# Optimization experiments

Measured on AMD Instinct MI355X. Metric: run time of the kernel, lower is better.

The kernel has to match this reference:

```python
import jax, jax.numpy as jnp
import numpy as np

GRID = 192
ISO = 0.0

CORNERS = [(0,0,0),(1,0,0),(0,1,0),(1,1,0),(0,0,1),(1,0,1),(0,1,1),(1,1,1)]
# 12 cube edges as pairs of corner offsets
EDGES = [
    ((0,0,0),(1,0,0)),((0,1,0),(1,1,0)),((0,0,1),(1,0,1)),((0,1,1),(1,1,1)),
    ((0,0,0),(0,1,0)),((1,0,0),(1,1,0)),((0,0,1),(0,1,1)),((1,0,1),(1,1,1)),
    ((0,0,0),(0,0,1)),((1,0,0),(1,0,1)),((0,1,0),(0,1,1)),((1,1,0),(1,1,1)),
]


def setup_inputs() -> dict:
    key = jax.random.key(0)
    grid = jax.random.normal(key, (GRID, GRID, GRID), dtype=jnp.float32)
    return {"grid": grid}


def _dual_verts(grid, iso):
    # One dual vertex per cell of the padded grid: mean of the iso-crossing
    # points on the cell's 12 edges (dual-marching-cubes vertex placement).
    X, Y, Z = grid.shape
    P = jnp.pad(grid, 1, constant_values=iso + 1.0)  # (X+2, Y+2, Z+2)
    Cx, Cy, Cz = X + 1, Y + 1, Z + 1                 # number of cells per axis
    vals = {c: P[c[0]:c[0]+Cx, c[1]:c[1]+Cy, c[2]:c[2]+Cz] for c in CORNERS}
    sum_pt = jnp.zeros((Cx, Cy, Cz, 3), grid.dtype)
    cnt = jnp.zeros((Cx, Cy, Cz), grid.dtype)
    for ca, cb in EDGES:  # fixed 12-iteration loop, fully vectorized over cells
        vA, vB = vals[ca], vals[cb]
        m = (vA < iso) != (vB < iso)                 # edge crosses isosurface
        t = jnp.where(m, (iso - vA) / jnp.where(m, vB - vA, 1.0), 0.0)
        oa = jnp.asarray(ca, grid.dtype)
        ob = jnp.asarray(cb, grid.dtype)
        pt = oa + t[..., None] * (ob - oa)           # local crossing point
        mf = m.astype(grid.dtype)
        sum_pt = sum_pt + mf[..., None] * pt
        cnt = cnt + mf
    base = jnp.stack(jnp.meshgrid(jnp.arange(Cx), jnp.arange(Cy), jnp.arange(Cz), indexing='ij'), axis=-1).astype(grid.dtype)
    verts = base + sum_pt / jnp.maximum(cnt, 1.0)[..., None]
    # undo +1 padding offset, then normalize by (dim - 1) as in the module
    verts = (verts - 1.0) / (jnp.asarray([X, Y, Z], grid.dtype) - 1.0)
    return verts.reshape(-1, 3), (cnt > 0).reshape(-1)


def _quads(grid, iso):
    # One quad per grid edge that crosses the isosurface, connecting the dual
    # vertices of the 4 cells sharing that edge. Emitted densely with a mask
    # (jit-compatible fixed shapes); masked rows are inactive.
    X, Y, Z = grid.shape
    P = jnp.pad(grid, 1, constant_values=iso + 1.0)
    Cx, Cy, Cz = X + 1, Y + 1, Z + 1
    sgn = P < iso
    def cid(a, b, c):  # flatten cell index
        return (a * Cy + b) * Cz + c
    qs, ms = [], []
    # x-directed edges: shared by cells (i, j-1/j, k-1/k)
    m = sgn[0:Cx, 1:Cy, 1:Cz] != sgn[1:Cx+1, 1:Cy, 1:Cz]
    a = jnp.arange(Cx)[:, None, None]; b = jnp.arange(1, Cy)[None, :, None]; c = jnp.arange(1, Cz)[None, None, :]
    q = jnp.stack(jnp.broadcast_arrays(cid(a, b-1, c-1), cid(a, b, c-1), cid(a, b, c), cid(a, b-1, c)), axis=-1)
    qs.append(q.reshape(-1, 4)); ms.append(m.reshape(-1))
    # y-directed edges: shared by cells (i-1/i, j, k-1/k)
    m = sgn[1:Cx, 0:Cy, 1:Cz] != sgn[1:Cx, 1:Cy+1, 1:Cz]
    a = jnp.arange(1, Cx)[:, None, None]; b = jnp.arange(Cy)[None, :, None]; c = jnp.arange(1, Cz)[None, None, :]
    q = jnp.stack(jnp.broadcast_arrays(cid(a-1, b, c-1), cid(a, b, c-1), cid(a, b, c), cid(a-1, b, c)), axis=-1)
    qs.append(q.reshape(-1, 4)); ms.append(m.reshape(-1))
    # z-directed edges: shared by cells (i-1/i, j-1/j, k)
    m = sgn[1:Cx, 1:Cy, 0:Cz] != sgn[1:Cx, 1:Cy, 1:Cz+1]
    a = jnp.arange(1, Cx)[:, None, None]; b = jnp.arange(1, Cy)[None, :, None]; c = jnp.arange(Cz)[None, None, :]
    q = jnp.stack(jnp.broadcast_arrays(cid(a-1, b-1, c), cid(a, b-1, c), cid(a, b, c), cid(a-1, b, c)), axis=-1)
    qs.append(q.reshape(-1, 4)); ms.append(m.reshape(-1))
    quads = jnp.concatenate(qs, axis=0).astype(jnp.int32)
    qmask = jnp.concatenate(ms, axis=0)
    return quads, qmask


def reference(grid):
    verts, vmask = _dual_verts(grid, ISO)
    quads, qmask = _quads(grid, ISO)
    return verts, vmask, quads, qmask
```

## Files before the change

kernel.cpp:

```cpp
#include <hip/hip_runtime.h>

#define GN 192
#define CN 193
#define CN2 (CN * CN)

#define NV        ((size_t)CN * CN * CN)
#define OFF_VMASK ((size_t)(NV * 3))
#define OFF_QUADS ((size_t)(OFF_VMASK + NV))
#define QSEG      ((size_t)CN * GN * GN)
#define OFF_QMASK ((size_t)(OFF_QUADS + 3 * QSEG * 4))

typedef float f4 __attribute__((ext_vector_type(4)));

__device__ __forceinline__ void nts(float* p, float v) { __builtin_nontemporal_store(v, p); }
__device__ __forceinline__ void nts4(f4* p, f4 v) { __builtin_nontemporal_store(v, p); }

#define QBLK 6948

__global__ __launch_bounds__(256) void dmc_quads(float* __restrict__ out) {
    f4* const quads = (f4*)(out + OFF_QUADS);
    const unsigned b = blockIdx.x;
    const unsigned seg = b / QBLK;
    const unsigned r0 = (b - seg * QBLK) * 1024u + threadIdx.x;
    float d0, d1, d2, d3;
    if (seg == 0)      { d0 = 0.f;      d1 = 193.f;  d2 = 194.f; d3 = 1.f; }
    else if (seg == 1) { d0 = -37249.f; d1 = 0.f;    d2 = 1.f;   d3 = -37248.f; }
    else               { d0 = -37442.f; d1 = -193.f; d2 = 0.f;   d3 = -37249.f; }
#pragma unroll
    for (int s = 0; s < 4; ++s) {
        const unsigned r = r0 + 256u * s;
        unsigned i, j, k, t;
        if (seg == 0)      { k = r % GN; t = r / GN; j = t % GN; i = t / GN; }
        else if (seg == 1) { k = r % GN; t = r / GN; j = t % CN; i = t / CN + 1; }
        else               { k = r % CN; t = r / CN; j = t % GN + 1; i = t / GN + 1; }
        const float flin = (float)((i * CN + j) * CN + k);
        nts4(quads + seg * QSEG + r, (f4){flin + d0, flin + d1, flin + d2, flin + d3});
    }
}

__global__ __launch_bounds__(256) void dmc_verts(const float* __restrict__ g,
                                                 float* __restrict__ out) {
    __shared__ __align__(16) float vlds[256 * 3];
    __shared__ float qAl[256], qBl[256], qCl[256];

    const int tid = threadIdx.x;
    const size_t lin0 = (size_t)blockIdx.x * 256;
    const size_t lin = lin0 + tid;
    const bool valid = lin < NV;
    const int linI = valid ? (int)lin : (int)(NV - 1);
    const int k = linI % CN;
    const int t2 = linI / CN;
    const int j = t2 % CN;
    const int i = t2 / CN;

    const int L0 = (int)lin0;
    const int L1 = (int)((lin0 + 255 < NV) ? (lin0 + 255) : (NV - 1));
    const int k0 = L0 % CN, u0 = L0 / CN, j0 = u0 % CN, i0 = u0 / CN;
    const int k1 = L1 % CN, u1 = L1 / CN, j1 = u1 % CN, i1 = u1 / CN;

    int rminA, rmaxA, rminB, rmaxB, rminC, rmaxC;
    { int a = i0, bb = j0, c = k0;
      if (bb == GN) { a++; bb = 0; c = 0; }
      else if (c == GN) { bb++; c = 0; if (bb == GN) { a++; bb = 0; } }
      rminA = (a * GN + bb) * GN + c; }
    { int a = i1, bb = j1, c = k1;
      if (bb == GN) { bb = GN - 1; c = GN - 1; }
      else if (c == GN) { c = GN - 1; }
      rmaxA = (a * GN + bb) * GN + c; }
    { int a = i0, bb = j0, c = k0;
      if (a == 0) { a = 1; bb = 0; c = 0; }
      else if (c == GN) { bb++; c = 0; if (bb == CN) { bb = 0; a++; } }
      rminB = ((a - 1) * CN + bb) * GN + c; }
    { int a = i1, bb = j1, c = k1;
      if (a == 0) rmaxB = -1;
      else { if (c == GN) c = GN - 1; rmaxB = ((a - 1) * CN + bb) * GN + c; } }
    { int a = i0, bb = j0, c = k0;
      if (a == 0) { a = 1; bb = 1; c = 0; }
      else if (bb == 0) { bb = 1; c = 0; }
      rminC = ((a - 1) * GN + (bb - 1)) * CN + c; }
    { int a = i1, bb = j1, c = k1;
      if (a == 0) rmaxC = -1;
      else if (bb == 0) { a--; rmaxC = (a == 0) ? -1 : ((a - 1) * GN + (GN - 1)) * CN + (CN - 1); }
      else rmaxC = ((a - 1) * GN + (bb - 1)) * CN + c; }
    int cntA = rmaxA - rminA + 1; if (cntA < 0) cntA = 0;
    int cntB = rmaxB - rminB + 1; if (cntB < 0) cntB = 0;
    int cntC = rmaxC - rminC + 1; if (cntC < 0) cntC = 0;

    const int xm = (i >= 1) ? i - 1 : 0;
    const int xp = (i <= GN - 1) ? i : GN - 1;
    const int ym = (j >= 1) ? j - 1 : 0;
    const int yp = (j <= GN - 1) ? j : GN - 1;
    const int zm = (k >= 1) ? k - 1 : 0;
    const int zp = (k <= GN - 1) ? k : GN - 1;
    const bool xv0 = (i >= 1), xv1 = (i <= GN - 1);
    const bool yv0 = (j >= 1), yv1 = (j <= GN - 1);
    const bool zv0 = (k >= 1), zv1 = (k <= GN - 1);

    const float* b00 = g + ((size_t)xm * GN + ym) * GN;
    const float* b01 = g + ((size_t)xm * GN + yp) * GN;
    const float* b10 = g + ((size_t)xp * GN + ym) * GN;
    const float* b11 = g + ((size_t)xp * GN + yp) * GN;

    const float v000 = (xv0 & yv0 & zv0) ? b00[zm] : 1.0f;
    const float v001 = (xv0 & yv0 & zv1) ? b00[zp] : 1.0f;
    const float v010 = (xv0 & yv1 & zv0) ? b01[zm] : 1.0f;
    const float v011 = (xv0 & yv1 & zv1) ? b01[zp] : 1.0f;
    const float v100 = (xv1 & yv0 & zv0) ? b10[zm] : 1.0f;
    const float v101 = (xv1 & yv0 & zv1) ? b10[zp] : 1.0f;
    const float v110 = (xv1 & yv1 & zv0) ? b11[zm] : 1.0f;
    const float v111 = (xv1 & yv1 & zv1) ? b11[zp] : 1.0f;

    float sx = 0.f, sy = 0.f, sz = 0.f, cf = 0.f;
    auto acc = [&](float vA, float vB, int axis, float o1, float o2) {
        const bool cr = (vA < 0.f) != (vB < 0.f);
        const float m = cr ? 1.0f : 0.0f;
        const float d = cr ? (vB - vA) : 1.0f;
        float r = __builtin_amdgcn_rcpf(d);
        r = r * (2.0f - d * r);
        const float t = cr ? (-vA * r) : 0.0f;
        if (axis == 0)      { sx += t;      sy += m * o1; sz += m * o2; }
        else if (axis == 1) { sx += m * o1; sy += t;      sz += m * o2; }
        else                { sx += m * o1; sy += m * o2; sz += t;      }
        cf += m;
    };
    acc(v000, v100, 0, 0.f, 0.f);
    acc(v010, v110, 0, 1.f, 0.f);
    acc(v001, v101, 0, 0.f, 1.f);
    acc(v011, v111, 0, 1.f, 1.f);
    acc(v000, v010, 1, 0.f, 0.f);
    acc(v100, v110, 1, 1.f, 0.f);
    acc(v001, v011, 1, 0.f, 1.f);
    acc(v101, v111, 1, 1.f, 1.f);
    acc(v000, v001, 2, 0.f, 0.f);
    acc(v100, v101, 2, 1.f, 0.f);
    acc(v010, v011, 2, 0.f, 1.f);
    acc(v110, v111, 2, 1.f, 1.f);

    const float cfm = fmaxf(cf, 1.0f);
    float rc = __builtin_amdgcn_rcpf(cfm);
    rc = rc * (2.0f - cfm * rc);
    const float inv191 = 1.0f / 191.0f;
    vlds[tid * 3 + 0] = ((float)i + sx * rc - 1.0f) * inv191;
    vlds[tid * 3 + 1] = ((float)j + sy * rc - 1.0f) * inv191;
    vlds[tid * 3 + 2] = ((float)k + sz * rc - 1.0f) * inv191;

    if (valid) nts(out + OFF_VMASK + lin, (cf > 0.f) ? 1.0f : 0.0f);

    if (valid) {
        if (j < GN && k < GN)
            qAl[(i * GN + j) * GN + k - rminA] = ((v011 < 0.f) != (v111 < 0.f)) ? 1.0f : 0.0f;
        if (i >= 1 && k < GN)
            qBl[((i - 1) * CN + j) * GN + k - rminB] = ((v001 < 0.f) != (v011 < 0.f)) ? 1.0f : 0.0f;
        if (i >= 1 && j >= 1)
            qCl[((i - 1) * GN + (j - 1)) * CN + k - rminC] = ((v000 < 0.f) != (v001 < 0.f)) ? 1.0f : 0.0f;
    }
    __syncthreads();

    const int nvalid = L1 - L0 + 1;
    const int nfl = 3 * nvalid;
    const int nf4 = nfl >> 2;
    if (tid < nf4)
        nts4((f4*)(out + lin0 * 3) + tid, ((const f4*)vlds)[tid]);
    if (tid == nf4)
        for (int rr = nf4 * 4; rr < nfl; ++rr) nts(out + lin0 * 3 + rr, vlds[rr]);

    if (tid < cntA) nts(out + OFF_QMASK + (size_t)rminA + tid, qAl[tid]);
    if (tid < cntB) nts(out + OFF_QMASK + QSEG + (size_t)rminB + tid, qBl[tid]);
    if (tid < cntC) nts(out + OFF_QMASK + 2 * QSEG + (size_t)rminC + tid, qCl[tid]);
}

extern "C" void kernel_launch(void* const* d_in, const int* in_sizes, int n_in,
                              void* d_out, int out_size, void* d_ws, size_t ws_size,
                              hipStream_t stream) {
    const float* g = (const float*)d_in[0];
    float* out = (float*)d_out;
    const int nbV = (int)((NV + 255) / 256);
    dmc_verts<<<dim3(nbV), dim3(256), 0, stream>>>(g, out);
    dmc_quads<<<dim3(3 * QBLK), dim3(256), 0, stream>>>(out);
}
```

Before: 573.5 us.

## Fuse vertex and quad kernels into persistent row-wise kernel with LDS double buffering

Replaces the separate vertex and quad kernels with one persistent kernel in which each block handles whole (i,j) rows of cells. The four input grid rows a row needs are staged into LDS with the next row prefetched into a second buffer, and vertices, masks, quad indices and quad masks are all written directly from that row. This removes the second launch, the redundant per-cell global gathers and the LDS repacking of mask outputs. In exchange, vertex output now uses scalar strided stores instead of packed float4 stores, and 256 threads cover only 193 cells, so about a quarter of the lanes sit idle in the compute phase.

```diff
diff --git a/kernel.cpp b/kernel.cpp
--- a/kernel.cpp
+++ b/kernel.cpp
@@ -2,7 +2,7 @@
 
 #define GN 192
 #define CN 193
-#define CN2 (CN * CN)
+#define NROWS (CN * CN)
 
 #define NV        ((size_t)CN * CN * CN)
 #define OFF_VMASK ((size_t)(NV * 3))
@@ -15,158 +15,125 @@
 __device__ __forceinline__ void nts(float* p, float v) { __builtin_nontemporal_store(v, p); }
 __device__ __forceinline__ void nts4(f4* p, f4 v) { __builtin_nontemporal_store(v, p); }
 
-#define QBLK 6948
+#define NBLK 4096
 
-__global__ __launch_bounds__(256) void dmc_quads(float* __restrict__ out) {
-    f4* const quads = (f4*)(out + OFF_QUADS);
-    const unsigned b = blockIdx.x;
-    const unsigned seg = b / QBLK;
-    const unsigned r0 = (b - seg * QBLK) * 1024u + threadIdx.x;
-    float d0, d1, d2, d3;
-    if (seg == 0)      { d0 = 0.f;      d1 = 193.f;  d2 = 194.f; d3 = 1.f; }
-    else if (seg == 1) { d0 = -37249.f; d1 = 0.f;    d2 = 1.f;   d3 = -37248.f; }
-    else               { d0 = -37442.f; d1 = -193.f; d2 = 0.f;   d3 = -37249.f; }
-#pragma unroll
-    for (int s = 0; s < 4; ++s) {
-        const unsigned r = r0 + 256u * s;
-        unsigned i, j, k, t;
-        if (seg == 0)      { k = r % GN; t = r / GN; j = t % GN; i = t / GN; }
-        else if (seg == 1) { k = r % GN; t = r / GN; j = t % CN; i = t / CN + 1; }
-        else               { k = r % CN; t = r / CN; j = t % GN + 1; i = t / GN + 1; }
-        const float flin = (float)((i * CN + j) * CN + k);
-        nts4(quads + seg * QSEG + r, (f4){flin + d0, flin + d1, flin + d2, flin + d3});
+__global__ __launch_bounds__(256) void dmc_rows(const float* __restrict__ g,
+                                                float* __restrict__ out) {
+    __shared__ float rows[2][4][194];
+    const int tid = threadIdx.x;
+
+    if (tid < 16) rows[tid >> 3][(tid >> 1) & 3][(tid & 1) * 193] = 1.0f;
+
+    const int  rsel   = tid / 48;
+    const int  f4i    = tid - rsel * 48;
+    const bool stager = tid < 192;
+
+    unsigned row = blockIdx.x;
+
+    if (row < NROWS && stager) {
+        const int i = row / CN, j = row - (row / CN) * CN;
+        const int gx = i - 1 + (rsel >> 1);
+        const int gy = j - 1 + (rsel & 1);
+        f4 v = (f4){1.f, 1.f, 1.f, 1.f};
+        if ((unsigned)gx < GN && (unsigned)gy < GN)
+            v = ((const f4*)(g + ((size_t)gx * GN + gy) * GN))[f4i];
+        float* d = &rows[0][rsel][1 + 4 * f4i];
+        d[0] = v.x; d[1] = v.y; d[2] = v.z; d[3] = v.w;
     }
-}
 
-__global__ __launch_bounds__(256) void dmc_verts(const float* __restrict__ g,
-                                                 float* __restrict__ out) {
-    __shared__ __align__(16) float vlds[256 * 3];
-    __shared__ float qAl[256], qBl[256], qCl[256];
+    int buf = 0;
+    for (; row < NROWS; row += NBLK) {
+        __syncthreads();
 
-    const int tid = threadIdx.x;
-    const size_t lin0 = (size_t)blockIdx.x * 256;
-    const size_t lin = lin0 + tid;
-    const bool valid = lin < NV;
-    const int linI = valid ? (int)lin : (int)(NV - 1);
-    const int k = linI % CN;
-    const int t2 = linI / CN;
-    const int j = t2 % CN;
-    const int i = t2 / CN;
+        const unsigned nrow = row + NBLK;
+        const bool havenext = (nrow < NROWS) && stager;
+        f4 nxt = (f4){1.f, 1.f, 1.f, 1.f};
+        if (havenext) {
+            const int ni = nrow / CN, nj = nrow - (nrow / CN) * CN;
+            const int gx = ni - 1 + (rsel >> 1);
+            const int gy = nj - 1 + (rsel & 1);
+            if ((unsigned)gx < GN && (unsigned)gy < GN)
+                nxt = ((const f4*)(g + ((size_t)gx * GN + gy) * GN))[f4i];
+        }
 
-    const int L0 = (int)lin0;
-    const int L1 = (int)((lin0 + 255 < NV) ? (lin0 + 255) : (NV - 1));
-    const int k0 = L0 % CN, u0 = L0 / CN, j0 = u0 % CN, i0 = u0 / CN;
-    const int k1 = L1 % CN, u1 = L1 / CN, j1 = u1 % CN, i1 = u1 / CN;
+        const int i = row / CN;
+        const int j = row - i * CN;
+        const int k = tid;
+        if (k < CN) {
+            const float* r00 = rows[buf][0];
+            const float* r01 = rows[buf][1];
+            const float* r10 = rows[buf][2];
+            const float* r11 = rows[buf][3];
+            const float v000 = r00[k], v001 = r00[k + 1];
+            const float v010 = r01[k], v011 = r01[k + 1];
+            const float v100 = r10[k], v101 = r10[k + 1];
+            const float v110 = r11[k], v111 = r11[k + 1];
 
-    int rminA, rmaxA, rminB, rmaxB, rminC, rmaxC;
-    { int a = i0, bb = j0, c = k0;
-      if (bb == GN) { a++; bb = 0; c = 0; }
-      else if (c == GN) { bb++; c = 0; if (bb == GN) { a++; bb = 0; } }
-      rminA = (a * GN + bb) * GN + c; }
-    { int a = i1, bb = j1, c = k1;
-      if (bb == GN) { bb = GN - 1; c = GN - 1; }
-      else if (c == GN) { c = GN - 1; }
-      rmaxA = (a * GN + bb) * GN + c; }
-    { int a = i0, bb = j0, c = k0;
-      if (a == 0) { a = 1; bb = 0; c = 0; }
-      else if (c == GN) { bb++; c = 0; if (bb == CN) { bb = 0; a++; } }
-      rminB = ((a - 1) * CN + bb) * GN + c; }
-    { int a = i1, bb = j1, c = k1;
-      if (a == 0) rmaxB = -1;
-      else { if (c == GN) c = GN - 1; rmaxB = ((a - 1) * CN + bb) * GN + c; } }
-    { int a = i0, bb = j0, c = k0;
-      if (a == 0) { a = 1; bb = 1; c = 0; }
-      else if (bb == 0) { bb = 1; c = 0; }
-      rminC = ((a - 1) * GN + (bb - 1)) * CN + c; }
-    { int a = i1, bb = j1, c = k1;
-      if (a == 0) rmaxC = -1;
-      else if (bb == 0) { a--; rmaxC = (a == 0) ? -1 : ((a - 1) * GN + (GN - 1)) * CN + (CN - 1); }
-      else rmaxC = ((a - 1) * GN + (bb - 1)) * CN + c; }
-    int cntA = rmaxA - rminA + 1; if (cntA < 0) cntA = 0;
-    int cntB = rmaxB - rminB + 1; if (cntB < 0) cntB = 0;
-    int cntC = rmaxC - rminC + 1; if (cntC < 0) cntC = 0;
+            float sx = 0.f, sy = 0.f, sz = 0.f, cf = 0.f;
+            auto acc = [&](float vA, float vB, int axis, float o1, float o2) {
+                const bool cr = (vA < 0.f) != (vB < 0.f);
+                const float m = cr ? 1.0f : 0.0f;
+                const float d = cr ? (vB - vA) : 1.0f;
+                float r = __builtin_amdgcn_rcpf(d);
+                r = r * (2.0f - d * r);
+                const float t = cr ? (-vA * r) : 0.0f;
+                if (axis == 0)      { sx += t;      sy += m * o1; sz += m * o2; }
+                else if (axis == 1) { sx += m * o1; sy += t;      sz += m * o2; }
+                else                { sx += m * o1; sy += m * o2; sz += t;      }
+                cf += m;
+            };
+            acc(v000, v100, 0, 0.f, 0.f);
+            acc(v010, v110, 0, 1.f, 0.f);
+            acc(v001, v101, 0, 0.f, 1.f);
+            acc(v011, v111, 0, 1.f, 1.f);
+            acc(v000, v010, 1, 0.f, 0.f);
+            acc(v100, v110, 1, 1.f, 0.f);
+            acc(v001, v011, 1, 0.f, 1.f);
+            acc(v101, v111, 1, 1.f, 1.f);
+            acc(v000, v001, 2, 0.f, 0.f);
+            acc(v100, v101, 2, 1.f, 0.f);
+            acc(v010, v011, 2, 0.f, 1.f);
+            acc(v110, v111, 2, 1.f, 1.f);
 
-    const int xm = (i >= 1) ? i - 1 : 0;
-    const int xp = (i <= GN - 1) ? i : GN - 1;
-    const int ym = (j >= 1) ? j - 1 : 0;
-    const int yp = (j <= GN - 1) ? j : GN - 1;
-    const int zm = (k >= 1) ? k - 1 : 0;
-    const int zp = (k <= GN - 1) ? k : GN - 1;
-    const bool xv0 = (i >= 1), xv1 = (i <= GN - 1);
-    const bool yv0 = (j >= 1), yv1 = (j <= GN - 1);
-    const bool zv0 = (k >= 1), zv1 = (k <= GN - 1);
+            const float cfm = fmaxf(cf, 1.0f);
+            float rc = __builtin_amdgcn_rcpf(cfm);
+            rc = rc * (2.0f - cfm * rc);
+            const float inv191 = 1.0f / 191.0f;
 
-    const float* b00 = g + ((size_t)xm * GN + ym) * GN;
-    const float* b01 = g + ((size_t)xm * GN + yp) * GN;
-    const float* b10 = g + ((size_t)xp * GN + ym) * GN;
-    const float* b11 = g + ((size_t)xp * GN + yp) * GN;
+            const int lin = (int)row * CN + k;
+            const float flin = (float)lin;
 
-    const float v000 = (xv0 & yv0 & zv0) ? b00[zm] : 1.0f;
-    const float v001 = (xv0 & yv0 & zv1) ? b00[zp] : 1.0f;
-    const float v010 = (xv0 & yv1 & zv0) ? b01[zm] : 1.0f;
-    const float v011 = (xv0 & yv1 & zv1) ? b01[zp] : 1.0f;
-    const float v100 = (xv1 & yv0 & zv0) ? b10[zm] : 1.0f;
-    const float v101 = (xv1 & yv0 & zv1) ? b10[zp] : 1.0f;
-    const float v110 = (xv1 & yv1 & zv0) ? b11[zm] : 1.0f;
-    const float v111 = (xv1 & yv1 & zv1) ? b11[zp] : 1.0f;
+            nts(out + (size_t)lin * 3 + 0, ((float)i + sx * rc - 1.0f) * inv191);
+            nts(out + (size_t)lin * 3 + 1, ((float)j + sy * rc - 1.0f) * inv191);
+            nts(out + (size_t)lin * 3 + 2, ((float)k + sz * rc - 1.0f) * inv191);
+            nts(out + OFF_VMASK + lin, (cf > 0.f) ? 1.0f : 0.0f);
 
-    float sx = 0.f, sy = 0.f, sz = 0.f, cf = 0.f;
-    auto acc = [&](float vA, float vB, int axis, float o1, float o2) {
-        const bool cr = (vA < 0.f) != (vB < 0.f);
-        const float m = cr ? 1.0f : 0.0f;
-        const float d = cr ? (vB - vA) : 1.0f;
-        float r = __builtin_amdgcn_rcpf(d);
-        r = r * (2.0f - d * r);
-        const float t = cr ? (-vA * r) : 0.0f;
-        if (axis == 0)      { sx += t;      sy += m * o1; sz += m * o2; }
-        else if (axis == 1) { sx += m * o1; sy += t;      sz += m * o2; }
-        else                { sx += m * o1; sy += m * o2; sz += t;      }
-        cf += m;
-    };
-    acc(v000, v100, 0, 0.f, 0.f);
-    acc(v010, v110, 0, 1.f, 0.f);
-    acc(v001, v101, 0, 0.f, 1.f);
-    acc(v011, v111, 0, 1.f, 1.f);
-    acc(v000, v010, 1, 0.f, 0.f);
-    acc(v100, v110, 1, 1.f, 0.f);
-    acc(v001, v011, 1, 0.f, 1.f);
-    acc(v101, v111, 1, 1.f, 1.f);
-    acc(v000, v001, 2, 0.f, 0.f);
-    acc(v100, v101, 2, 1.f, 0.f);
-    acc(v010, v011, 2, 0.f, 1.f);
-    acc(v110, v111, 2, 1.f, 1.f);
+            f4* const quads = (f4*)(out + OFF_QUADS);
+            float* const qmask = out + OFF_QMASK;
 
-    const float cfm = fmaxf(cf, 1.0f);
-    float rc = __builtin_amdgcn_rcpf(cfm);
-    rc = rc * (2.0f - cfm * rc);
-    const float inv191 = 1.0f / 191.0f;
-    vlds[tid * 3 + 0] = ((float)i + sx * rc - 1.0f) * inv191;
-    vlds[tid * 3 + 1] = ((float)j + sy * rc - 1.0f) * inv191;
-    vlds[tid * 3 + 2] = ((float)k + sz * rc - 1.0f) * inv191;
+            if (j < GN && k < GN) {
+                const size_t rA = ((size_t)i * GN + j) * GN + k;
+                nts4(quads + rA, (f4){flin, flin + 193.f, flin + 194.f, flin + 1.f});
+                nts(qmask + rA, ((v011 < 0.f) != (v111 < 0.f)) ? 1.0f : 0.0f);
+            }
+            if (i >= 1 && k < GN) {
+                const size_t rB = QSEG + ((size_t)(i - 1) * CN + j) * GN + k;
+                nts4(quads + rB, (f4){flin - 37249.f, flin, flin + 1.f, flin - 37248.f});
+                nts(qmask + rB, ((v001 < 0.f) != (v011 < 0.f)) ? 1.0f : 0.0f);
+            }
+            if (i >= 1 && j >= 1) {
+                const size_t rC = 2 * QSEG + ((size_t)(i - 1) * GN + (j - 1)) * CN + k;
+                nts4(quads + rC, (f4){flin - 37442.f, flin - 193.f, flin, flin - 37249.f});
+                nts(qmask + rC, ((v000 < 0.f) != (v001 < 0.f)) ? 1.0f : 0.0f);
+            }
+        }
 
-    if (valid) nts(out + OFF_VMASK + lin, (cf > 0.f) ? 1.0f : 0.0f);
-
-    if (valid) {
-        if (j < GN && k < GN)
-            qAl[(i * GN + j) * GN + k - rminA] = ((v011 < 0.f) != (v111 < 0.f)) ? 1.0f : 0.0f;
-        if (i >= 1 && k < GN)
-            qBl[((i - 1) * CN + j) * GN + k - rminB] = ((v001 < 0.f) != (v011 < 0.f)) ? 1.0f : 0.0f;
-        if (i >= 1 && j >= 1)
-            qCl[((i - 1) * GN + (j - 1)) * CN + k - rminC] = ((v000 < 0.f) != (v001 < 0.f)) ? 1.0f : 0.0f;
+        if (havenext) {
+            float* d = &rows[buf ^ 1][rsel][1 + 4 * f4i];
+            d[0] = nxt.x; d[1] = nxt.y; d[2] = nxt.z; d[3] = nxt.w;
+        }
+        buf ^= 1;
     }
-    __syncthreads();
-
-    const int nvalid = L1 - L0 + 1;
-    const int nfl = 3 * nvalid;
-    const int nf4 = nfl >> 2;
-    if (tid < nf4)
-        nts4((f4*)(out + lin0 * 3) + tid, ((const f4*)vlds)[tid]);
-    if (tid == nf4)
-        for (int rr = nf4 * 4; rr < nfl; ++rr) nts(out + lin0 * 3 + rr, vlds[rr]);
-
-    if (tid < cntA) nts(out + OFF_QMASK + (size_t)rminA + tid, qAl[tid]);
-    if (tid < cntB) nts(out + OFF_QMASK + QSEG + (size_t)rminB + tid, qBl[tid]);
-    if (tid < cntC) nts(out + OFF_QMASK + 2 * QSEG + (size_t)rminC + tid, qCl[tid]);
 }
 
 extern "C" void kernel_launch(void* const* d_in, const int* in_sizes, int n_in,
@@ -174,7 +141,5 @@
                               hipStream_t stream) {
     const float* g = (const float*)d_in[0];
     float* out = (float*)d_out;
-    const int nbV = (int)((NV + 255) / 256);
-    dmc_verts<<<dim3(nbV), dim3(256), 0, stream>>>(g, out);
-    dmc_quads<<<dim3(3 * QBLK), dim3(256), 0, stream>>>(out);
+    dmc_rows<<<dim3(NBLK), dim3(256), 0, stream>>>(g, out);
 }
```

Measured after the change: 612.5 us. +6.8%, slower.
